# Kernel tuning notes

Hardware: AMD Instinct MI355X
Metric: run time of the kernel (lower is better)

## Reference

```python
import jax, jax.numpy as jnp
import numpy as np

B, S, D, F, E = 8, 8192, 256, 1024, 8
ROUTE_KEY = 42  # fixed seed replacing torch's Categorical(...).sample()


def setup_inputs() -> dict:
    key = jax.random.key(0)
    ks = jax.random.split(key, 8)
    scale = 0.02
    return {
        "x": jax.random.normal(ks[0], (B, S, D), dtype=jnp.float32),
        "gate_w": jax.random.normal(ks[1], (D, E), dtype=jnp.float32) * scale,
        "gate_b": jnp.zeros((E,), dtype=jnp.float32),
        "w1": jax.random.normal(ks[2], (E, D, F), dtype=jnp.float32) * scale,
        "b1": jnp.zeros((E, F), dtype=jnp.float32),
        "w2": jax.random.normal(ks[3], (E, F, D), dtype=jnp.float32) * scale,
        "b2": jnp.zeros((E, D), dtype=jnp.float32),
    }


def reference(x, gate_w, gate_b, w1, b1, w2, b2):
    # Gate: logits -> softmax -> sample one expert per token.
    # (softmax is monotonic-preserving for categorical sampling, so sampling
    # from logits directly matches Categorical(softmax(logits)).sample().)
    gate_logits = jnp.einsum("bsd,de->bse", x, gate_w) + gate_b
    chosen = jax.random.categorical(jax.random.key(ROUTE_KEY), gate_logits)  # [B,S] int

    num_experts = w1.shape[0]
    out = jnp.zeros_like(x)
    for e in range(num_experts):  # small fixed expert count
        h = jax.nn.relu(jnp.einsum("bsd,df->bsf", x, w1[e]) + b1[e])
        y = jnp.einsum("bsf,fd->bsd", h, w2[e]) + b2[e]
        # scatter-write rows routed to expert e (dropout is identity in eval)
        out = out + jnp.where((chosen == e)[..., None], y, jnp.zeros((), x.dtype))
    return out
```

## Files before the change

### kernel.cpp

```cpp
#include <hip/hip_runtime.h>
#include <hip/hip_bf16.h>

#define NTOK 65536
#define DD 256
#define FF 1024
#define EE 8
#define BSTRIDE 12288
#define MTILE 64
#define NTILES (BSTRIDE / MTILE)
#define CHUNK_US 16384

typedef short bh8 __attribute__((ext_vector_type(8)));
typedef float f4v __attribute__((ext_vector_type(4)));

__device__ __forceinline__ unsigned rotl32(unsigned v, int d) {
  return (v << d) | (v >> (32 - d));
}

__device__ __forceinline__ unsigned jax_random_bits32(unsigned c0, unsigned c1) {
  const unsigned k0 = 0u, k1 = 42u;
  const unsigned k2 = 0x1BD11BDAu ^ k0 ^ k1;
  unsigned x0 = c0 + k0, x1 = c1 + k1;
#define TFR(r) { x0 += x1; x1 = rotl32(x1, (r)); x1 ^= x0; }
  TFR(13) TFR(15) TFR(26) TFR(6)
  x0 += k1; x1 += k2 + 1u;
  TFR(17) TFR(29) TFR(16) TFR(24)
  x0 += k2; x1 += k0 + 2u;
  TFR(13) TFR(15) TFR(26) TFR(6)
  x0 += k0; x1 += k1 + 3u;
  TFR(17) TFR(29) TFR(16) TFR(24)
  x0 += k1; x1 += k2 + 4u;
  TFR(13) TFR(15) TFR(26) TFR(6)
  x0 += k2; x1 += k0 + 5u;
#undef TFR
  return x0 ^ x1;
}

__device__ __forceinline__ ushort f2bf(float f) {
  union { float f; unsigned u; } c; c.f = f;
  unsigned r = c.u + 0x7fffu + ((c.u >> 16) & 1u);
  return (ushort)(r >> 16);
}

__device__ __forceinline__ unsigned pack2(float a, float b) {
  return (unsigned)f2bf(a) | ((unsigned)f2bf(b) << 16);
}

__global__ __launch_bounds__(1024) void gate_route3(
    const float* __restrict__ x, const float* __restrict__ gw,
    const float* __restrict__ gb, int* __restrict__ counts,
    int* __restrict__ buckets, ushort* __restrict__ xbf) {
  __shared__ float gwt[EE * DD];
  __shared__ int hist[EE], sbase[EE];
  __shared__ unsigned char chs[64];
  __shared__ short lps[64];

  const int tid = threadIdx.x;
  if (tid < EE) hist[tid] = 0;
  for (int i = tid; i < DD * EE; i += 1024) {
    const int d = i >> 3, e = i & 7;
    gwt[e * DD + d] = gw[i];
  }
  __syncthreads();

  const int lane = tid & 63;
  const int wave = tid >> 6;
  const int grp = lane >> 4;
  const int gl = lane & 15;
  const int slot = wave * 4 + grp;
  const int t = blockIdx.x * 64 + slot;

  float acc[EE] = {0.f, 0.f, 0.f, 0.f, 0.f, 0.f, 0.f, 0.f};
  const float* xr = x + (size_t)t * DD;
#pragma unroll
  for (int j = 0; j < 4; ++j) {
    const int d0 = j * 64 + gl * 4;
    const float4 xv = *reinterpret_cast<const float4*>(xr + d0);
    if (xbf != nullptr) {
      ushort4 xb;
      xb.x = f2bf(xv.x); xb.y = f2bf(xv.y); xb.z = f2bf(xv.z); xb.w = f2bf(xv.w);
      *reinterpret_cast<ushort4*>(xbf + (size_t)t * DD + d0) = xb;
    }
#pragma unroll
    for (int e = 0; e < EE; ++e) {
      const float4 g = *reinterpret_cast<const float4*>(&gwt[e * DD + d0]);
      acc[e] = fmaf(xv.x, g.x, acc[e]);
      acc[e] = fmaf(xv.y, g.y, acc[e]);
      acc[e] = fmaf(xv.z, g.z, acc[e]);
      acc[e] = fmaf(xv.w, g.w, acc[e]);
    }
  }
#pragma unroll
  for (int off = 8; off >= 1; off >>= 1)
#pragma unroll
    for (int e = 0; e < EE; ++e) acc[e] += __shfl_xor(acc[e], off);

  const int e = gl & 7;
  float logit = 0.f;
#pragma unroll
  for (int q = 0; q < EE; ++q) logit = (e == q) ? acc[q] : logit;
  logit += gb[e];

  const unsigned bits = jax_random_bits32(0u, (unsigned)(t * EE + e));
  const float f = __uint_as_float((bits >> 9) | 0x3f800000u) - 1.0f;
  const float u = fmaxf(1.17549435e-38f, f);
  float val = -logf(-logf(u)) + logit;
  int idx = e;
#pragma unroll
  for (int off = 4; off > 0; off >>= 1) {
    const float ov = __shfl_xor(val, off);
    const int oi = __shfl_xor(idx, off);
    if (ov > val || (ov == val && oi < idx)) { val = ov; idx = oi; }
  }
  if (gl == 0) {
    const int lp = atomicAdd(&hist[idx], 1);
    chs[slot] = (unsigned char)idx;
    lps[slot] = (short)lp;
  }
  __syncthreads();
  if (tid < EE) sbase[tid] = atomicAdd(&counts[tid], hist[tid]);
  __syncthreads();
  if (tid < 64) {
    const int ee = chs[tid];
    const int p = sbase[ee] + lps[tid];
    if (p < BSTRIDE) buckets[ee * BSTRIDE + p] = blockIdx.x * 64 + tid;
  }
}

__global__ __launch_bounds__(256) void prep_w1s(
    const float* __restrict__ w1, ushort* __restrict__ w1s) {
  __shared__ float ts[64][65];
  const int e = blockIdx.z;
  const int f0 = blockIdx.x * 64, d0 = blockIdx.y * 64;
  const int tx = threadIdx.x, ty = threadIdx.y;
  const float* s = w1 + (size_t)e * DD * FF;
  char* dimg = (char*)(w1s + (size_t)e * 16 * CHUNK_US + blockIdx.x * CHUNK_US);
#pragma unroll
  for (int i = 0; i < 16; ++i)
    ts[ty * 16 + i][tx] = s[(size_t)(d0 + ty * 16 + i) * FF + f0 + tx];
  __syncthreads();
#pragma unroll
  for (int i = 0; i < 16; ++i) {
    const int fl = ty * 16 + i;
    const int byte = ((fl * 512 + (d0 + tx) * 2)) ^ ((fl & 31) << 4);
    *reinterpret_cast<ushort*>(dimg + byte) = f2bf(ts[tx][fl]);
  }
}

__global__ __launch_bounds__(256) void prep_w2s(
    const float* __restrict__ w2, ushort* __restrict__ w2s) {
  __shared__ float ts[64][65];
  const int e = blockIdx.z;
  const int d0 = blockIdx.x * 64, f0 = blockIdx.y * 64;
  const int tx = threadIdx.x, ty = threadIdx.y;
  const float* s = w2 + (size_t)e * FF * DD;
  char* dimg = (char*)(w2s + (size_t)e * 16 * CHUNK_US + blockIdx.y * CHUNK_US);
#pragma unroll
  for (int i = 0; i < 16; ++i)
    ts[ty * 16 + i][tx] = s[(size_t)(f0 + ty * 16 + i) * DD + d0 + tx];
  __syncthreads();
#pragma unroll
  for (int i = 0; i < 16; ++i) {
    const int d = d0 + ty * 16 + i;
    const int byte = ((d * 128 + tx * 2)) ^ ((d & 31) << 4);
    *reinterpret_cast<ushort*>(dimg + byte) = f2bf(ts[tx][ty * 16 + i]);
  }
}

__device__ __forceinline__ void stage32k(const ushort* g, ushort* l, int wid, int lane) {
  const ushort* gs = g + wid * 2048 + lane * 8;
  ushort* ls = l + wid * 2048;
#pragma unroll
  for (int i = 0; i < 4; ++i)
    __builtin_amdgcn_global_load_lds(
        (const __attribute__((address_space(1))) void*)(gs + i * 512),
        (__attribute__((address_space(3))) void*)(ls + i * 512), 16, 0, 0);
}

__global__ __launch_bounds__(512, 4) void ffn_mfma10(
    const ushort* __restrict__ xbf, const ushort* __restrict__ w1s,
    const float* __restrict__ b1, const ushort* __restrict__ w2s,
    const float* __restrict__ b2, const int* __restrict__ counts,
    const int* __restrict__ buckets, float* __restrict__ out) {
  const int e = blockIdx.x & 7;
  const int tile = blockIdx.x >> 3;
  const int cnt = min(counts[e], BSTRIDE);
  const int m0 = tile * MTILE;
  if (m0 >= cnt) return;

  __shared__ ushort W1b[CHUNK_US];
  __shared__ ushort W2b[CHUNK_US];
  __shared__ ushort Hb[4096];

  const int tid = threadIdx.x;
  const int lane = tid & 63;
  const int wid = tid >> 6;
  const int l15 = lane & 15;
  const int q = lane >> 4;
  const int fp = wid >> 2;
  const int mt = wid & 3;
  const int dh = wid >> 2;

  const ushort* w1g = w1s + (size_t)e * 16 * CHUNK_US;
  const ushort* w2g = w2s + (size_t)e * 16 * CHUNK_US;

  stage32k(w1g, W1b, wid, lane);
  stage32k(w2g, W2b, wid, lane);

  const int mxi = m0 + mt * 16 + l15;
  const int tokx = buckets[e * BSTRIDE + (mxi < cnt ? mxi : cnt - 1)];
  const ushort* xp = xbf + (size_t)tokx * DD + q * 8;
  bh8 xf[8];
#pragma unroll
  for (int dks = 0; dks < 8; ++dks)
    xf[dks] = *reinterpret_cast<const bh8*>(xp + dks * 32);

  __syncthreads();

  f4v yacc[8] = {};

#pragma unroll 1
  for (int c = 0; c < 16; ++c) {
    {
      const char* wb = reinterpret_cast<const char*>(W1b);
      f4v h0 = {}, h1 = {};
      const int fl0 = (2 * fp) * 16 + l15;
      const int fl1 = (2 * fp + 1) * 16 + l15;
#pragma unroll
      for (int dks = 0; dks < 8; ++dks) {
        const int co = (32 * dks + 8 * q) * 2;
        const bh8 a0 = *reinterpret_cast<const bh8*>(
            wb + ((fl0 * 512 + co) ^ ((fl0 & 31) << 4)));
        const bh8 a1 = *reinterpret_cast<const bh8*>(
            wb + ((fl1 * 512 + co) ^ ((fl1 & 31) << 4)));
        h0 = __builtin_amdgcn_mfma_f32_16x16x32_bf16(a0, xf[dks], h0, 0, 0, 0);
        h1 = __builtin_amdgcn_mfma_f32_16x16x32_bf16(a1, xf[dks], h1, 0, 0, 0);
      }
      char* hbb = reinterpret_cast<char*>(Hb);
#pragma unroll
      for (int th = 0; th < 2; ++th) {
        const int t = 2 * fp + th;
        const float4 bv = *reinterpret_cast<const float4*>(
            b1 + e * FF + c * 64 + t * 16 + 4 * q);
        const f4v& ha = th ? h1 : h0;
        const float v0 = fmaxf(ha[0] + bv.x, 0.f);
        const float v1 = fmaxf(ha[1] + bv.y, 0.f);
        const float v2 = fmaxf(ha[2] + bv.z, 0.f);
        const float v3 = fmaxf(ha[3] + bv.w, 0.f);
        const int laneT = (2 * th + (q >> 1)) * 16 + l15;
        const int base = ((mt * 2 + fp) * 64 + laneT) * 16;
        *reinterpret_cast<unsigned*>(hbb + base + (((2 * q + 0) & 3) << 2)) = pack2(v0, v1);
        *reinterpret_cast<unsigned*>(hbb + base + (((2 * q + 1) & 3) << 2)) = pack2(v2, v3);
      }
    }
    __syncthreads();

    if (c < 15)
      stage32k(w1g + (size_t)(c + 1) * CHUNK_US, W1b, wid, lane);

    {
      const char* hbb = reinterpret_cast<const char*>(Hb);
      const char* wb = reinterpret_cast<const char*>(W2b);
#pragma unroll
      for (int ks = 0; ks < 2; ++ks) {
        const bh8 af = *reinterpret_cast<const bh8*>(
            hbb + ((mt * 2 + ks) * 64 + lane) * 16);
        const int co = (32 * ks + 8 * q) * 2;
#pragma unroll
        for (int dt = 0; dt < 8; ++dt) {
          const int d = (dh * 8 + dt) * 16 + l15;
          const bh8 b = *reinterpret_cast<const bh8*>(
              wb + ((d * 128 + co) ^ ((d & 31) << 4)));
          yacc[dt] = __builtin_amdgcn_mfma_f32_16x16x32_bf16(af, b, yacc[dt], 0, 0, 0);
        }
      }
    }
    __syncthreads();

    if (c < 15)
      stage32k(w2g + (size_t)(c + 1) * CHUNK_US, W2b, wid, lane);
  }

  int toks4[4];
#pragma unroll
  for (int r = 0; r < 4; ++r) {
    const int m = m0 + mt * 16 + 4 * q + r;
    toks4[r] = buckets[e * BSTRIDE + (m < cnt ? m : cnt - 1)];
  }
#pragma unroll
  for (int dt = 0; dt < 8; ++dt) {
    const int d = (dh * 8 + dt) * 16 + l15;
    const float b2v = b2[e * DD + d];
#pragma unroll
    for (int r = 0; r < 4; ++r) {
      const int m = mt * 16 + 4 * q + r;
      if (m0 + m < cnt)
        out[(size_t)toks4[r] * DD + d] = yacc[dt][r] + b2v;
    }
  }
}

__global__ __launch_bounds__(512) void ffn_fp32(
    const float* __restrict__ x, const float* __restrict__ w1,
    const float* __restrict__ b1, const float* __restrict__ w2,
    const float* __restrict__ b2, const int* __restrict__ counts,
    const int* __restrict__ buckets, float* __restrict__ out, int bstride) {
  const int e = blockIdx.y;
  const int cnt = min(counts[e], bstride);
  const int m0 = blockIdx.x * 64;
  if (m0 >= cnt) return;

  __shared__ float Xt[DD][64];
  __shared__ float Ht[64][64];
  __shared__ int toks[64];

  const int tid = threadIdx.x;
  if (tid < 64) {
    const int i = m0 + tid;
    toks[tid] = buckets[e * bstride + (i < cnt ? i : cnt - 1)];
  }
  __syncthreads();

  for (int idx = tid; idx < 64 * (DD / 4); idx += 512) {
    const int r = idx >> 6;
    const int c4 = idx & 63;
    const float4 v = *reinterpret_cast<const float4*>(x + (size_t)toks[r] * DD + c4 * 4);
    Xt[c4 * 4 + 0][r] = v.x;
    Xt[c4 * 4 + 1][r] = v.y;
    Xt[c4 * 4 + 2][r] = v.z;
    Xt[c4 * 4 + 3][r] = v.w;
  }
  __syncthreads();

  const int fg = tid & 15;
  const int mg = tid >> 4;
  const int dc = tid & 63;
  const int mgrp = tid >> 6;

  float yacc[8][4];
#pragma unroll
  for (int i = 0; i < 8; ++i)
#pragma unroll
    for (int jj = 0; jj < 4; ++jj) yacc[i][jj] = 0.f;

  for (int fc0 = 0; fc0 < FF; fc0 += 64) {
    float hacc[2][4];
#pragma unroll
    for (int i = 0; i < 2; ++i)
#pragma unroll
      for (int jj = 0; jj < 4; ++jj) hacc[i][jj] = 0.f;

    const float* w1p = w1 + (size_t)e * DD * FF + fc0 + fg * 4;
    for (int d = 0; d < DD; ++d) {
      const float4 w = *reinterpret_cast<const float4*>(w1p + (size_t)d * FF);
      const float2 xv = *reinterpret_cast<const float2*>(&Xt[d][mg * 2]);
      const float ws[4] = {w.x, w.y, w.z, w.w};
      const float xl[2] = {xv.x, xv.y};
#pragma unroll
      for (int i = 0; i < 2; ++i)
#pragma unroll
        for (int jj = 0; jj < 4; ++jj)
          hacc[i][jj] = fmaf(xl[i], ws[jj], hacc[i][jj]);
    }
#pragma unroll
    for (int jj = 0; jj < 4; ++jj) {
      const float bb = b1[e * FF + fc0 + fg * 4 + jj];
      Ht[fg * 4 + jj][mg * 2 + 0] = fmaxf(hacc[0][jj] + bb, 0.f);
      Ht[fg * 4 + jj][mg * 2 + 1] = fmaxf(hacc[1][jj] + bb, 0.f);
    }
    __syncthreads();

    const float* w2p = w2 + (size_t)e * FF * DD + (size_t)fc0 * DD + dc * 4;
    for (int f = 0; f < 64; ++f) {
      const float4 w = *reinterpret_cast<const float4*>(w2p + (size_t)f * DD);
      const float4 h0 = *reinterpret_cast<const float4*>(&Ht[f][mgrp * 8]);
      const float4 h1 = *reinterpret_cast<const float4*>(&Ht[f][mgrp * 8 + 4]);
      const float hs[8] = {h0.x, h0.y, h0.z, h0.w, h1.x, h1.y, h1.z, h1.w};
      const float ws[4] = {w.x, w.y, w.z, w.w};
#pragma unroll
      for (int i = 0; i < 8; ++i)
#pragma unroll
        for (int jj = 0; jj < 4; ++jj)
          yacc[i][jj] = fmaf(hs[i], ws[jj], yacc[i][jj]);
    }
    __syncthreads();
  }

#pragma unroll
  for (int i = 0; i < 8; ++i) {
    const int r = mgrp * 8 + i;
    if (m0 + r < cnt) {
      float4 o;
      o.x = yacc[i][0] + b2[e * DD + dc * 4 + 0];
      o.y = yacc[i][1] + b2[e * DD + dc * 4 + 1];
      o.z = yacc[i][2] + b2[e * DD + dc * 4 + 2];
      o.w = yacc[i][3] + b2[e * DD + dc * 4 + 3];
      *reinterpret_cast<float4*>(out + (size_t)toks[r] * DD + dc * 4) = o;
    }
  }
}

extern "C" void kernel_launch(void* const* d_in, const int* in_sizes, int n_in,
                              void* d_out, int out_size, void* d_ws, size_t ws_size,
                              hipStream_t stream) {
  const float* x  = (const float*)d_in[0];
  const float* gw = (const float*)d_in[1];
  const float* gb = (const float*)d_in[2];
  const float* w1 = (const float*)d_in[3];
  const float* b1 = (const float*)d_in[4];
  const float* w2 = (const float*)d_in[5];
  const float* b2 = (const float*)d_in[6];
  float* out = (float*)d_out;

  int* counts = (int*)d_ws;
  int* buckets = (int*)((char*)d_ws + 4096);
  ushort* w1s = (ushort*)((char*)d_ws + 524288);
  ushort* w2s = (ushort*)((char*)d_ws + 524288 + 4194304);
  ushort* xbf = (ushort*)((char*)d_ws + 524288 + 2ull * 4194304);
  const size_t need = 524288 + 2ull * 4194304 + (size_t)NTOK * DD * 2;

  hipMemsetAsync(d_ws, 0, 4096, stream);

  if (ws_size >= need) {
    hipLaunchKernelGGL(gate_route3, dim3(NTOK / 64), dim3(1024), 0, stream,
                       x, gw, gb, counts, buckets, xbf);
    hipLaunchKernelGGL(prep_w1s, dim3(FF / 64, DD / 64, EE), dim3(64, 4), 0, stream,
                       w1, w1s);
    hipLaunchKernelGGL(prep_w2s, dim3(DD / 64, FF / 64, EE), dim3(64, 4), 0, stream,
                       w2, w2s);
    hipLaunchKernelGGL(ffn_mfma10, dim3(NTILES * EE), dim3(512), 0, stream,
                       xbf, w1s, b1, w2s, b2, counts, buckets, out);
  } else {
    hipLaunchKernelGGL(gate_route3, dim3(NTOK / 64), dim3(1024), 0, stream,
                       x, gw, gb, counts, buckets, (ushort*)nullptr);
    hipLaunchKernelGGL(ffn_fp32, dim3(NTOK / 64, EE), dim3(512), 0, stream,
                       x, w1, b1, w2, b2, counts, buckets, out, BSTRIDE);
  }
}
```

Before: 168.0 us.

## Double token tile per block to reuse staged expert weight chunks

Raises the per-block token tile from 64 to 128 rows, so each wave now computes two 16-row sub-tiles against every staged W1/W2 chunk. Each weight chunk loaded into LDS then feeds twice as many MFMAs, which halves the weight staging traffic per token. The cost is twice the accumulator registers, a larger H buffer, and a launch bound lowered to 2 blocks per CU. Fewer and larger blocks also mean more padding waste on experts with few tokens.

```diff
diff --git a/kernel.cpp b/kernel.cpp
--- a/kernel.cpp
+++ b/kernel.cpp
@@ -6,7 +6,7 @@
 #define FF 1024
 #define EE 8
 #define BSTRIDE 12288
-#define MTILE 64
+#define MTILE 128
 #define NTILES (BSTRIDE / MTILE)
 #define CHUNK_US 16384
 
@@ -177,7 +177,7 @@
         (__attribute__((address_space(3))) void*)(ls + i * 512), 16, 0, 0);
 }
 
-__global__ __launch_bounds__(512, 4) void ffn_mfma10(
+__global__ __launch_bounds__(512, 2) void ffn_mfma11(
     const ushort* __restrict__ xbf, const ushort* __restrict__ w1s,
     const float* __restrict__ b1, const ushort* __restrict__ w2s,
     const float* __restrict__ b2, const int* __restrict__ counts,
@@ -190,7 +190,8 @@
 
   __shared__ ushort W1b[CHUNK_US];
   __shared__ ushort W2b[CHUNK_US];
-  __shared__ ushort Hb[4096];
+  __shared__ ushort Hb[8192];
+  __shared__ int toks[MTILE];
 
   const int tid = threadIdx.x;
   const int lane = tid & 63;
@@ -198,8 +199,13 @@
   const int l15 = lane & 15;
   const int q = lane >> 4;
   const int fp = wid >> 2;
-  const int mt = wid & 3;
+  const int mg = wid & 3;
   const int dh = wid >> 2;
+
+  if (tid < MTILE) {
+    const int i = m0 + tid;
+    toks[tid] = buckets[e * BSTRIDE + (i < cnt ? i : cnt - 1)];
+  }
 
   const ushort* w1g = w1s + (size_t)e * 16 * CHUNK_US;
   const ushort* w2g = w2s + (size_t)e * 16 * CHUNK_US;
@@ -207,34 +213,39 @@
   stage32k(w1g, W1b, wid, lane);
   stage32k(w2g, W2b, wid, lane);
 
-  const int mxi = m0 + mt * 16 + l15;
-  const int tokx = buckets[e * BSTRIDE + (mxi < cnt ? mxi : cnt - 1)];
-  const ushort* xp = xbf + (size_t)tokx * DD + q * 8;
-  bh8 xf[8];
-#pragma unroll
-  for (int dks = 0; dks < 8; ++dks)
-    xf[dks] = *reinterpret_cast<const bh8*>(xp + dks * 32);
-
-  __syncthreads();
-
-  f4v yacc[8] = {};
+  bh8 xf[2][8];
+#pragma unroll
+  for (int i = 0; i < 2; ++i) {
+    const int mxi = m0 + (mg + 4 * i) * 16 + l15;
+    const int tokx = buckets[e * BSTRIDE + (mxi < cnt ? mxi : cnt - 1)];
+    const ushort* xp = xbf + (size_t)tokx * DD + q * 8;
+#pragma unroll
+    for (int dks = 0; dks < 8; ++dks)
+      xf[i][dks] = *reinterpret_cast<const bh8*>(xp + dks * 32);
+  }
+
+  __syncthreads();
+
+  f4v yacc[2][8] = {};
 
 #pragma unroll 1
   for (int c = 0; c < 16; ++c) {
     {
       const char* wb = reinterpret_cast<const char*>(W1b);
-      f4v h0 = {}, h1 = {};
+      f4v hacc[2][2] = {};
       const int fl0 = (2 * fp) * 16 + l15;
       const int fl1 = (2 * fp + 1) * 16 + l15;
 #pragma unroll
       for (int dks = 0; dks < 8; ++dks) {
-        const int co = (32 * dks + 8 * q) * 2;
+        const int co = 64 * dks + 16 * q;
         const bh8 a0 = *reinterpret_cast<const bh8*>(
             wb + ((fl0 * 512 + co) ^ ((fl0 & 31) << 4)));
         const bh8 a1 = *reinterpret_cast<const bh8*>(
             wb + ((fl1 * 512 + co) ^ ((fl1 & 31) << 4)));
-        h0 = __builtin_amdgcn_mfma_f32_16x16x32_bf16(a0, xf[dks], h0, 0, 0, 0);
-        h1 = __builtin_amdgcn_mfma_f32_16x16x32_bf16(a1, xf[dks], h1, 0, 0, 0);
+        hacc[0][0] = __builtin_amdgcn_mfma_f32_16x16x32_bf16(a0, xf[0][dks], hacc[0][0], 0, 0, 0);
+        hacc[0][1] = __builtin_amdgcn_mfma_f32_16x16x32_bf16(a0, xf[1][dks], hacc[0][1], 0, 0, 0);
+        hacc[1][0] = __builtin_amdgcn_mfma_f32_16x16x32_bf16(a1, xf[0][dks], hacc[1][0], 0, 0, 0);
+        hacc[1][1] = __builtin_amdgcn_mfma_f32_16x16x32_bf16(a1, xf[1][dks], hacc[1][1], 0, 0, 0);
       }
       char* hbb = reinterpret_cast<char*>(Hb);
 #pragma unroll
@@ -242,15 +253,21 @@
         const int t = 2 * fp + th;
         const float4 bv = *reinterpret_cast<const float4*>(
             b1 + e * FF + c * 64 + t * 16 + 4 * q);
-        const f4v& ha = th ? h1 : h0;
-        const float v0 = fmaxf(ha[0] + bv.x, 0.f);
-        const float v1 = fmaxf(ha[1] + bv.y, 0.f);
-        const float v2 = fmaxf(ha[2] + bv.z, 0.f);
-        const float v3 = fmaxf(ha[3] + bv.w, 0.f);
-        const int laneT = (2 * th + (q >> 1)) * 16 + l15;
-        const int base = ((mt * 2 + fp) * 64 + laneT) * 16;
-        *reinterpret_cast<unsigned*>(hbb + base + (((2 * q + 0) & 3) << 2)) = pack2(v0, v1);
-        *reinterpret_cast<unsigned*>(hbb + base + (((2 * q + 1) & 3) << 2)) = pack2(v2, v3);
+#pragma unroll
+        for (int i = 0; i < 2; ++i) {
+          const f4v& ha = hacc[th][i];
+          const float v0 = fmaxf(ha[0] + bv.x, 0.f);
+          const float v1 = fmaxf(ha[1] + bv.y, 0.f);
+          const float v2 = fmaxf(ha[2] + bv.z, 0.f);
+          const float v3 = fmaxf(ha[3] + bv.w, 0.f);
+          const int mt = mg + 4 * i;
+          const int laneT = (2 * th + (q >> 1)) * 16 + l15;
+          const int base = ((mt * 2 + fp) * 64 + laneT) * 16;
+          uint2 wv;
+          wv.x = pack2(v0, v1);
+          wv.y = pack2(v2, v3);
+          *reinterpret_cast<uint2*>(hbb + base + ((q & 1) << 3)) = wv;
+        }
       }
     }
     __syncthreads();
@@ -263,15 +280,21 @@
       const char* wb = reinterpret_cast<const char*>(W2b);
 #pragma unroll
       for (int ks = 0; ks < 2; ++ks) {
-        const bh8 af = *reinterpret_cast<const bh8*>(
-            hbb + ((mt * 2 + ks) * 64 + lane) * 16);
-        const int co = (32 * ks + 8 * q) * 2;
+        bh8 af[2];
+#pragma unroll
+        for (int i2 = 0; i2 < 2; ++i2) {
+          const int mt = mg + 4 * i2;
+          af[i2] = *reinterpret_cast<const bh8*>(
+              hbb + ((mt * 2 + ks) * 64 + lane) * 16);
+        }
+        const int co = (ks * 32 + 8 * q) * 2;
 #pragma unroll
         for (int dt = 0; dt < 8; ++dt) {
           const int d = (dh * 8 + dt) * 16 + l15;
           const bh8 b = *reinterpret_cast<const bh8*>(
               wb + ((d * 128 + co) ^ ((d & 31) << 4)));
-          yacc[dt] = __builtin_amdgcn_mfma_f32_16x16x32_bf16(af, b, yacc[dt], 0, 0, 0);
+          yacc[0][dt] = __builtin_amdgcn_mfma_f32_16x16x32_bf16(af[0], b, yacc[0][dt], 0, 0, 0);
+          yacc[1][dt] = __builtin_amdgcn_mfma_f32_16x16x32_bf16(af[1], b, yacc[1][dt], 0, 0, 0);
         }
       }
     }
@@ -281,21 +304,19 @@
       stage32k(w2g + (size_t)(c + 1) * CHUNK_US, W2b, wid, lane);
   }
 
-  int toks4[4];
-#pragma unroll
-  for (int r = 0; r < 4; ++r) {
-    const int m = m0 + mt * 16 + 4 * q + r;
-    toks4[r] = buckets[e * BSTRIDE + (m < cnt ? m : cnt - 1)];
-  }
-#pragma unroll
-  for (int dt = 0; dt < 8; ++dt) {
-    const int d = (dh * 8 + dt) * 16 + l15;
-    const float b2v = b2[e * DD + d];
-#pragma unroll
-    for (int r = 0; r < 4; ++r) {
-      const int m = mt * 16 + 4 * q + r;
-      if (m0 + m < cnt)
-        out[(size_t)toks4[r] * DD + d] = yacc[dt][r] + b2v;
+#pragma unroll
+  for (int i2 = 0; i2 < 2; ++i2) {
+    const int mt = mg + 4 * i2;
+#pragma unroll
+    for (int dt = 0; dt < 8; ++dt) {
+      const int d = (dh * 8 + dt) * 16 + l15;
+      const float b2v = b2[e * DD + d];
+#pragma unroll
+      for (int r = 0; r < 4; ++r) {
+        const int m = mt * 16 + 4 * q + r;
+        if (m0 + m < cnt)
+          out[(size_t)toks[m] * DD + d] = yacc[i2][dt][r] + b2v;
+      }
     }
   }
 }
@@ -428,7 +449,7 @@
                        w1, w1s);
     hipLaunchKernelGGL(prep_w2s, dim3(DD / 64, FF / 64, EE), dim3(64, 4), 0, stream,
                        w2, w2s);
-    hipLaunchKernelGGL(ffn_mfma10, dim3(NTILES * EE), dim3(512), 0, stream,
+    hipLaunchKernelGGL(ffn_mfma11, dim3(NTILES * EE), dim3(512), 0, stream,
                        xbf, w1s, b1, w2s, b2, counts, buckets, out);
   } else {
     hipLaunchKernelGGL(gate_route3, dim3(NTOK / 64), dim3(1024), 0, stream,
```

Result: slower. 187.1 us (+11.4%).

## Split fused expert FFN into two GEMM kernels via bf16 hidden buffer

Applied to the files above, without the earlier changes.

Replaces the single fused FFN kernel with two launches. The first computes relu(xW1+b1) for each expert over a 2D grid (token tile × F chunk) and writes a bf16 hidden matrix to workspace. The second streams double-buffered W2 chunks into LDS and reduces over F for 64-token tiles. The aim is more parallelism and better occupancy than the fused per-tile loop over F. The cost is about 128MB of extra global traffic for writing and rereading H, plus a new workspace requirement; the fused path remains as a fallback.

```diff
diff --git a/kernel.cpp b/kernel.cpp
--- a/kernel.cpp
+++ b/kernel.cpp
@@ -6,8 +6,6 @@
 #define FF 1024
 #define EE 8
 #define BSTRIDE 12288
-#define MTILE 64
-#define NTILES (BSTRIDE / MTILE)
 #define CHUNK_US 16384
 
 typedef short bh8 __attribute__((ext_vector_type(8)));
@@ -177,6 +175,149 @@
         (__attribute__((address_space(3))) void*)(ls + i * 512), 16, 0, 0);
 }
 
+__global__ __launch_bounds__(512, 4) void gemm1_split(
+    const ushort* __restrict__ xbf, const ushort* __restrict__ w1s,
+    const float* __restrict__ b1, const int* __restrict__ counts,
+    const int* __restrict__ buckets, ushort* __restrict__ H) {
+  const int e = blockIdx.x & 7;
+  const int tile = blockIdx.x >> 3;
+  const int fc = blockIdx.y;
+  const int cnt = min(counts[e], BSTRIDE);
+  const int m0 = tile * 128;
+  if (m0 >= cnt) return;
+
+  __shared__ ushort W1b[CHUNK_US];
+
+  const int tid = threadIdx.x;
+  const int lane = tid & 63;
+  const int wid = tid >> 6;
+  const int l15 = lane & 15;
+  const int q = lane >> 4;
+  const int fp = wid >> 2;
+  const int mg = wid & 3;
+
+  stage32k(w1s + ((size_t)e * 16 + fc) * CHUNK_US, W1b, wid, lane);
+
+  int tokx[2];
+  bh8 xf[2][8];
+#pragma unroll
+  for (int i = 0; i < 2; ++i) {
+    const int mxi = m0 + (mg + 4 * i) * 16 + l15;
+    tokx[i] = buckets[e * BSTRIDE + (mxi < cnt ? mxi : cnt - 1)];
+    const ushort* xp = xbf + (size_t)tokx[i] * DD + q * 8;
+#pragma unroll
+    for (int dks = 0; dks < 8; ++dks)
+      xf[i][dks] = *reinterpret_cast<const bh8*>(xp + dks * 32);
+  }
+
+  __syncthreads();
+
+  const char* wb = reinterpret_cast<const char*>(W1b);
+  f4v hacc[2][2] = {};
+  const int fl0 = (2 * fp) * 16 + l15;
+  const int fl1 = (2 * fp + 1) * 16 + l15;
+#pragma unroll
+  for (int dks = 0; dks < 8; ++dks) {
+    const int co = 64 * dks + 16 * q;
+    const bh8 a0 = *reinterpret_cast<const bh8*>(
+        wb + ((fl0 * 512 + co) ^ ((fl0 & 31) << 4)));
+    const bh8 a1 = *reinterpret_cast<const bh8*>(
+        wb + ((fl1 * 512 + co) ^ ((fl1 & 31) << 4)));
+    hacc[0][0] = __builtin_amdgcn_mfma_f32_16x16x32_bf16(a0, xf[0][dks], hacc[0][0], 0, 0, 0);
+    hacc[0][1] = __builtin_amdgcn_mfma_f32_16x16x32_bf16(a0, xf[1][dks], hacc[0][1], 0, 0, 0);
+    hacc[1][0] = __builtin_amdgcn_mfma_f32_16x16x32_bf16(a1, xf[0][dks], hacc[1][0], 0, 0, 0);
+    hacc[1][1] = __builtin_amdgcn_mfma_f32_16x16x32_bf16(a1, xf[1][dks], hacc[1][1], 0, 0, 0);
+  }
+
+#pragma unroll
+  for (int th = 0; th < 2; ++th) {
+    const int ft = 2 * fp + th;
+    const float4 bv = *reinterpret_cast<const float4*>(
+        b1 + e * FF + fc * 64 + ft * 16 + 4 * q);
+#pragma unroll
+    for (int i = 0; i < 2; ++i) {
+      const f4v& ha = hacc[th][i];
+      uint2 wv;
+      wv.x = pack2(fmaxf(ha[0] + bv.x, 0.f), fmaxf(ha[1] + bv.y, 0.f));
+      wv.y = pack2(fmaxf(ha[2] + bv.z, 0.f), fmaxf(ha[3] + bv.w, 0.f));
+      *reinterpret_cast<uint2*>(
+          H + (size_t)tokx[i] * FF + fc * 64 + ft * 16 + 4 * q) = wv;
+    }
+  }
+}
+
+__global__ __launch_bounds__(512, 4) void gemm2_split(
+    const ushort* __restrict__ H, const ushort* __restrict__ w2s,
+    const float* __restrict__ b2, const int* __restrict__ counts,
+    const int* __restrict__ buckets, float* __restrict__ out) {
+  const int e = blockIdx.x & 7;
+  const int tile = blockIdx.x >> 3;
+  const int cnt = min(counts[e], BSTRIDE);
+  const int m0 = tile * 64;
+  if (m0 >= cnt) return;
+
+  __shared__ ushort W2b[2][CHUNK_US];
+  __shared__ int toks[64];
+
+  const int tid = threadIdx.x;
+  const int lane = tid & 63;
+  const int wid = tid >> 6;
+  const int l15 = lane & 15;
+  const int q = lane >> 4;
+  const int mh = wid >> 1;
+  const int dh = wid & 1;
+
+  if (tid < 64) {
+    const int i = m0 + tid;
+    toks[tid] = buckets[e * BSTRIDE + (i < cnt ? i : cnt - 1)];
+  }
+
+  const ushort* w2g = w2s + (size_t)e * 16 * CHUNK_US;
+  stage32k(w2g, W2b[0], wid, lane);
+
+  const int mxi = m0 + mh * 16 + l15;
+  const int tokA = buckets[e * BSTRIDE + (mxi < cnt ? mxi : cnt - 1)];
+  const ushort* hp = H + (size_t)tokA * FF + q * 8;
+
+  __syncthreads();
+
+  f4v yacc[8] = {};
+
+#pragma unroll 1
+  for (int fc = 0; fc < 16; ++fc) {
+    const int p = fc & 1;
+    if (fc < 15)
+      stage32k(w2g + (size_t)(fc + 1) * CHUNK_US, W2b[p ^ 1], wid, lane);
+
+    const char* wb = reinterpret_cast<const char*>(W2b[p]);
+#pragma unroll
+    for (int ks = 0; ks < 2; ++ks) {
+      const bh8 af = *reinterpret_cast<const bh8*>(hp + fc * 64 + ks * 32);
+      const int co = ks * 64 + q * 16;
+#pragma unroll
+      for (int dt = 0; dt < 8; ++dt) {
+        const int d = dh * 128 + dt * 16 + l15;
+        const bh8 b = *reinterpret_cast<const bh8*>(
+            wb + ((d * 128 + co) ^ ((d & 31) << 4)));
+        yacc[dt] = __builtin_amdgcn_mfma_f32_16x16x32_bf16(af, b, yacc[dt], 0, 0, 0);
+      }
+    }
+    __syncthreads();
+  }
+
+#pragma unroll
+  for (int dt = 0; dt < 8; ++dt) {
+    const int d = dh * 128 + dt * 16 + l15;
+    const float b2v = b2[e * DD + d];
+#pragma unroll
+    for (int r = 0; r < 4; ++r) {
+      const int m = mh * 16 + 4 * q + r;
+      if (m0 + m < cnt)
+        out[(size_t)toks[m] * DD + d] = yacc[dt][r] + b2v;
+    }
+  }
+}
+
 __global__ __launch_bounds__(512, 4) void ffn_mfma10(
     const ushort* __restrict__ xbf, const ushort* __restrict__ w1s,
     const float* __restrict__ b1, const ushort* __restrict__ w2s,
@@ -185,7 +326,7 @@
   const int e = blockIdx.x & 7;
   const int tile = blockIdx.x >> 3;
   const int cnt = min(counts[e], BSTRIDE);
-  const int m0 = tile * MTILE;
+  const int m0 = tile * 64;
   if (m0 >= cnt) return;
 
   __shared__ ushort W1b[CHUNK_US];
@@ -417,19 +558,28 @@
   ushort* w1s = (ushort*)((char*)d_ws + 524288);
   ushort* w2s = (ushort*)((char*)d_ws + 524288 + 4194304);
   ushort* xbf = (ushort*)((char*)d_ws + 524288 + 2ull * 4194304);
-  const size_t need = 524288 + 2ull * 4194304 + (size_t)NTOK * DD * 2;
+  ushort* H   = (ushort*)((char*)d_ws + 524288 + 2ull * 4194304 + 33554432);
+  const size_t need_mid = 524288 + 2ull * 4194304 + 33554432;
+  const size_t need_big = need_mid + (size_t)NTOK * FF * 2;
 
   hipMemsetAsync(d_ws, 0, 4096, stream);
 
-  if (ws_size >= need) {
+  if (ws_size >= need_mid) {
     hipLaunchKernelGGL(gate_route3, dim3(NTOK / 64), dim3(1024), 0, stream,
                        x, gw, gb, counts, buckets, xbf);
     hipLaunchKernelGGL(prep_w1s, dim3(FF / 64, DD / 64, EE), dim3(64, 4), 0, stream,
                        w1, w1s);
     hipLaunchKernelGGL(prep_w2s, dim3(DD / 64, FF / 64, EE), dim3(64, 4), 0, stream,
                        w2, w2s);
-    hipLaunchKernelGGL(ffn_mfma10, dim3(NTILES * EE), dim3(512), 0, stream,
-                       xbf, w1s, b1, w2s, b2, counts, buckets, out);
+    if (ws_size >= need_big) {
+      hipLaunchKernelGGL(gemm1_split, dim3((BSTRIDE / 128) * EE, 16), dim3(512), 0, stream,
+                         xbf, w1s, b1, counts, buckets, H);
+      hipLaunchKernelGGL(gemm2_split, dim3((BSTRIDE / 64) * EE), dim3(512), 0, stream,
+                         H, w2s, b2, counts, buckets, out);
+    } else {
+      hipLaunchKernelGGL(ffn_mfma10, dim3((BSTRIDE / 64) * EE), dim3(512), 0, stream,
+                         xbf, w1s, b1, w2s, b2, counts, buckets, out);
+    }
   } else {
     hipLaunchKernelGGL(gate_route3, dim3(NTOK / 64), dim3(1024), 0, stream,
                        x, gw, gb, counts, buckets, (ushort*)nullptr);
```

Result: slower. 302.7 us (+80.2%).
